# Kernel optimization log

Hardware: AMD Instinct MI355X
Metric: run time of the kernel (lower is better)

The kernel has to match this reference:

```python
import jax, jax.numpy as jnp
import numpy as np

N = 8192          # number of samples
L_FIT = 1.0       # fit (ridge) kernel lengthscale (l_scale folded in)
L_MMD = 1.0       # mmd kernel lengthscale (l_scale folded in)
NUGGET = 1e-4     # diagonal nugget added before inversion
REG_LAMBDA = 1e-5 # regularization weight


def rbf(A, B, l):
    """RBF Gram matrix: exp(-||a-b||^2 / (2 l^2)). A:[n,d], B:[m,d] -> [n,m]."""
    d2 = (jnp.sum(A * A, axis=1)[:, None]
          + jnp.sum(B * B, axis=1)[None, :]
          - 2.0 * (A @ B.T))
    d2 = jnp.maximum(d2, 0.0)
    return jnp.exp(-d2 / (2.0 * l * l))


def setup_inputs() -> dict:
    key = jax.random.key(0)
    k1, k2, k3, k4 = jax.random.split(key, 4)
    X_mu = jax.random.normal(k1, (N, 2), dtype=jnp.float32)
    Y_eta = jax.random.normal(k2, (N, 2), dtype=jnp.float32)
    Y_mu = jax.random.normal(k3, (N, 2), dtype=jnp.float32)
    Z = jax.random.normal(k4, (N, 2), dtype=jnp.float32)  # transport parameter
    return {"X_mu": X_mu, "Y_eta": Y_eta, "Y_mu": Y_mu, "Z": Z}


def reference(X_mu, Y_eta, Y_mu, Z):
    # loss_mmd: MMD between mapped samples and target, uniform weights 1/N
    map_vec = jnp.concatenate([X_mu, Y_eta + Z], axis=1)  # [N, dx+dy]
    Y = jnp.concatenate([X_mu, Y_mu], axis=1)             # [N, dx+dy]
    Ek_ZZ = jnp.mean(rbf(map_vec, map_vec, L_MMD))  # alpha^T K alpha with alpha=1/N
    Ek_ZY = jnp.mean(rbf(map_vec, Y, L_MMD))
    Ek_YY = jnp.mean(rbf(Y, Y, L_MMD))               # E_mmd_YY (constant in torch code)
    loss_mmd = Ek_ZZ - 2.0 * Ek_ZY + Ek_YY

    # loss_reg: reg_lambda * trace(Z^T (K_XX + nugget I)^{-1} Z)
    X = jnp.concatenate([X_mu, Y_eta], axis=1)
    K_fit = rbf(X, X, L_FIT) + NUGGET * jnp.eye(N, dtype=X.dtype)
    K_inv = jnp.linalg.inv(K_fit)
    loss_reg = REG_LAMBDA * jnp.sum(Z * (K_inv @ Z))  # = trace(Z^T Kinv Z)

    return loss_mmd + loss_reg
```

## Files before the change

kernel.cpp:

```cpp
#include <hip/hip_runtime.h>

#define NPTS 8192
#define N2 (NPTS * 2)
#define NCH 16
#define JCH (NPTS / NCH)
#define ITILE 256
#define NIT (NPTS / ITILE)
#define NBLK1 (NIT * NCH)
#define IB 8
#define NIG (ITILE / IB)
#define NJS 16
#define JPT (JCH / NJS)
#define MNY 512
#define SSTR 16
#define T_ITERS 144
#define NUG 1.0e-4
#define INVNUG 1.0e4
#define DELTA 1.0e-2
#define LAM 1.0e-5

#if __has_builtin(__builtin_amdgcn_exp2f)
#define EXP2F(x) __builtin_amdgcn_exp2f(x)
#else
#define EXP2F(x) __expf(0.6931471805599453f * (x))
#endif

extern "C" __global__ void __launch_bounds__(256)
k_setup(const float* __restrict__ Xmu, const float* __restrict__ Yeta,
        const float* __restrict__ Ymu, const float* __restrict__ Z,
        float4* __restrict__ U4, float4* __restrict__ W4, float* __restrict__ NS,
        float4* __restrict__ M4, float4* __restrict__ Y4,
        float2* __restrict__ Pf0, float2* __restrict__ Pf1,
        double* __restrict__ r64, double* __restrict__ x64)
{
  const float c2 = 0.84932180028802f;
  int tid = threadIdx.x;
  int idx = blockIdx.x * 256 + tid;
  int i = idx >> 1;
  r64[idx] = (double)Z[idx];
  x64[idx] = 0.0;
  if ((idx & 1) == 0) {
    float a0 = Xmu[2 * i], a1 = Xmu[2 * i + 1];
    float e0 = Yeta[2 * i], e1 = Yeta[2 * i + 1];
    float m0 = Ymu[2 * i], m1 = Ymu[2 * i + 1];
    float z0 = Z[2 * i], z1 = Z[2 * i + 1];
    float u0 = c2 * a0, u1 = c2 * a1, u2 = c2 * e0, u3 = c2 * e1;
    float n = fmaf(u3, u3, fmaf(u2, u2, fmaf(u1, u1, u0 * u0)));
    U4[i] = make_float4(u0, u1, u2, u3);
    W4[i] = make_float4(2.f * u0, 2.f * u1, 2.f * u2, 2.f * u3);
    NS[i] = n;
    M4[i] = make_float4(a0, a1, e0 + z0, e1 + z1);
    Y4[i] = make_float4(a0, a1, m0, m1);
    Pf0[i] = make_float2(0.f, 0.f);
    Pf1[i] = make_float2(0.f, 0.f);
  }
}

#define MTPB 256
#define MCH 1024
extern "C" __global__ void __launch_bounds__(MTPB)
k_mmd(const float4* __restrict__ M4, const float4* __restrict__ Y4,
      double* __restrict__ mmdpart)
{
  __shared__ float4 sM[MCH];
  __shared__ float4 sY[MCH];
  __shared__ double sred[MTPB];
  int tid = threadIdx.x;
  int blk = blockIdx.x;
  int itile = blk >> 3;
  int ch = blk & 7;
  int j0 = ch * MCH;
  for (int u = tid; u < MCH; u += MTPB) {
    sM[u] = M4[j0 + u];
    sY[u] = Y4[j0 + u];
  }
  __syncthreads();
  int i = itile * MTPB + tid;
  float4 mi = M4[i];
  float4 yi = Y4[i];
  double szz = 0.0, szy = 0.0, syy = 0.0;
  for (int jj = 0; jj < MCH; ++jj) {
    float4 mj = sM[jj];
    float4 yj = sY[jj];
    float d0 = mi.x - mj.x, d1 = mi.y - mj.y;
    float a = fmaf(d1, d1, d0 * d0);
    float u0 = mi.z - mj.z, u1 = mi.w - mj.w;
    float v0 = mi.z - yj.z, v1 = mi.w - yj.w;
    float w0 = yi.z - yj.z, w1 = yi.w - yj.w;
    float dzz = fmaf(u0, u0, fmaf(u1, u1, a));
    float dzy = fmaf(v0, v0, fmaf(v1, v1, a));
    float dyy = fmaf(w0, w0, fmaf(w1, w1, a));
    szz += (double)__expf(-0.5f * dzz);
    szy += (double)__expf(-0.5f * dzy);
    syy += (double)__expf(-0.5f * dyy);
  }
  double v[3] = {szz, szy, syy};
  for (int k = 0; k < 3; ++k) {
    sred[tid] = v[k];
    __syncthreads();
    for (int st = MTPB >> 1; st >= 1; st >>= 1) {
      if (tid < st) sred[tid] += sred[tid + st];
      __syncthreads();
    }
    if (tid == 0) mmdpart[blk * 3 + k] = sred[0];
    __syncthreads();
  }
}

__device__ __forceinline__ float evalK(float4 u, float nu, float4 ws, float nss) {
  float tt = fmaf(u.x, ws.x, fmaf(u.y, ws.y, fmaf(u.z, ws.z, u.w * ws.w)));
  return EXP2F(tt - nu - nss);
}

extern "C" __global__ void __launch_bounds__(256)
k_gbuild(const float4* __restrict__ U4, const float4* __restrict__ W4,
         const float* __restrict__ NS, double* __restrict__ G)
{
  __shared__ float ea[8][32];
  __shared__ float eb[8][32];
  int tid = threadIdx.x;
  int blk = blockIdx.x;
  int a0 = (blk >> 4) * 32;
  int b0 = (blk & 15) * 32;
  int arow = tid >> 5;
  int bl = tid & 31;
  int sa = (a0 + bl) * SSTR;
  int sb = (b0 + bl) * SSTR;
  float4 wsa = W4[sa]; float nsa = NS[sa];
  float4 wsb = W4[sb]; float nsb = NS[sb];
  double acc[4] = {0.0, 0.0, 0.0, 0.0};
  for (int ic = 0; ic < NPTS / 8; ++ic) {
    int i = ic * 8 + arow;
    float4 u = U4[i];
    float nu = NS[i];
    ea[arow][bl] = evalK(u, nu, wsa, nsa);
    eb[arow][bl] = evalK(u, nu, wsb, nsb);
    __syncthreads();
#pragma unroll
    for (int kk = 0; kk < 4; ++kk) {
      int al = (tid >> 5) + 8 * kk;
      double s = 0.0;
#pragma unroll
      for (int ii = 0; ii < 8; ++ii)
        s += (double)ea[ii][al] * (double)eb[ii][bl];
      acc[kk] += s;
    }
    __syncthreads();
  }
#pragma unroll
  for (int kk = 0; kk < 4; ++kk) {
    int al = (tid >> 5) + 8 * kk;
    int a = a0 + al, b = b0 + bl;
    int ia = a * SSTR;
    float4 ua = U4[ia];
    float na = NS[ia];
    double w_ab = (double)evalK(ua, na, wsb, nsb);
    double g = acc[kk] + NUG * w_ab + ((a == b) ? DELTA : 0.0);
    G[(size_t)a * MNY + b] = g;
  }
}

extern "C" __global__ void __launch_bounds__(512)
k_gjpanel(const double* __restrict__ Mc, double* __restrict__ Mn, int k0)
{
  __shared__ double pm[8][8];
  __shared__ double sW[8][MNY];
  __shared__ double cl[8][8];
  __shared__ double trow[8], tcol[8];
  __shared__ double ps;
  int tid = threadIdx.x;
  int blk = blockIdx.x;

  if (tid < 64)
    pm[tid >> 3][tid & 7] = Mc[(size_t)(k0 + (tid >> 3)) * MNY + k0 + (tid & 7)];
  __syncthreads();
  for (int piv = 0; piv < 8; ++piv) {
    if (tid == 0) ps = 1.0 / pm[piv][piv];
    if (tid < 8) { trow[tid] = pm[piv][tid]; tcol[tid] = pm[tid][piv]; }
    __syncthreads();
    double p = ps;
    if (tid < 64) {
      int r = tid >> 3, c = tid & 7;
      double v;
      if (r == piv && c == piv) v = p;
      else if (r == piv)        v = trow[c] * p;
      else if (c == piv)        v = -tcol[r] * p;
      else                      v = fma(-tcol[r] * p, trow[c], pm[r][c]);
      pm[r][c] = v;
    }
    __syncthreads();
  }
  {
    double m[8];
#pragma unroll
    for (int s = 0; s < 8; ++s) m[s] = Mc[(size_t)(k0 + s) * MNY + tid];
#pragma unroll
    for (int r = 0; r < 8; ++r) {
      double acc = 0.0;
#pragma unroll
      for (int s = 0; s < 8; ++s) acc = fma(pm[r][s], m[s], acc);
      sW[r][tid] = acc;
    }
  }
  if (tid < 64)
    cl[tid >> 3][tid & 7] = Mc[(size_t)(blk * 8 + (tid >> 3)) * MNY + k0 + (tid & 7)];
  __syncthreads();

  bool ownerPanel = (blk == (k0 >> 3));
  int jk = tid - k0;
  bool inK = (jk >= 0 && jk < 8);
#pragma unroll
  for (int rr = 0; rr < 8; ++rr) {
    int i = blk * 8 + rr;
    double v;
    if (ownerPanel) {
      v = inK ? pm[rr][jk] : sW[rr][tid];
    } else if (inK) {
      double acc = 0.0;
#pragma unroll
      for (int s = 0; s < 8; ++s) acc = fma(cl[rr][s], pm[s][jk], acc);
      v = -acc;
    } else {
      double acc = Mc[(size_t)i * MNY + tid];
#pragma unroll
      for (int s = 0; s < 8; ++s) acc = fma(-cl[rr][s], sW[s][tid], acc);
      v = acc;
    }
    Mn[(size_t)i * MNY + tid] = v;
  }
}

extern "C" __global__ void __launch_bounds__(512)
k_dbuild(const float4* __restrict__ U4, const float4* __restrict__ W4,
         const float* __restrict__ NS, const double* __restrict__ Ginv,
         float* __restrict__ D)
{
  __shared__ float sc[16][MNY];
  __shared__ float4 su[16];
  __shared__ float snl[16];
  int tid = threadIdx.x;
  int blk = blockIdx.x;
  int i0 = blk * 16;
  if (tid < 16) { su[tid] = U4[i0 + tid]; snl[tid] = NS[i0 + tid]; }
  __syncthreads();
  {
    int si = tid * SSTR;
    float4 ws = W4[si];
    float nss = NS[si];
#pragma unroll
    for (int r = 0; r < 16; ++r)
      sc[r][tid] = evalK(su[r], snl[r], ws, nss);
  }
  __syncthreads();
  double acc[16];
#pragma unroll
  for (int r = 0; r < 16; ++r) acc[r] = 0.0;
  for (int k = 0; k < MNY; ++k) {
    double g = Ginv[(size_t)k * MNY + tid];
#pragma unroll
    for (int r = 0; r < 16; ++r)
      acc[r] = fma((double)sc[r][k], g, acc[r]);
  }
#pragma unroll
  for (int r = 0; r < 16; ++r)
    D[(size_t)(i0 + r) * MNY + tid] = (float)acc[r];
}

extern "C" __global__ void __launch_bounds__(512, 4)
k_matvec(const float4* __restrict__ U4, const float4* __restrict__ W4,
         const float* __restrict__ NS,
         const float2* __restrict__ Zv, const float2* __restrict__ Pfp,
         float2* __restrict__ Pfc, float2* __restrict__ qpart,
         double* __restrict__ pqpart, const double* __restrict__ rhopart, int t)
{
  __shared__ float4 sw[JCH];
  __shared__ float4 sa[JCH];
  __shared__ double s1[512], s2[512];
  __shared__ double sc[2];
  int tid = threadIdx.x;
  int blk = blockIdx.x;
  int it = blk >> 4;
  int ch = blk & (NCH - 1);
  int j = ch * JCH + tid;

  float4 wj = W4[j];
  float nj = NS[j];
  float2 zj = Zv[j];
  float2 pj = Pfp[j];

  if (t == 1) {
    if (tid < 2) sc[tid] = 0.0;
    __syncthreads();
  } else {
    const double* cur = rhopart + ((t - 1) & 1) * 128;
    const double* prv = rhopart + ((t - 2) & 1) * 128;
    if (tid < 128) { s1[tid] = cur[tid]; s2[tid] = prv[tid]; }
    __syncthreads();
    for (int st = 64; st >= 2; st >>= 1) {
      if (tid < st) { s1[tid] += s1[tid + st]; s2[tid] += s2[tid + st]; }
      __syncthreads();
    }
    if (tid < 2) sc[tid] = s1[tid] / s2[tid];
    __syncthreads();
  }
  float b0 = (float)sc[0], b1 = (float)sc[1];

  sw[tid] = wj;
  sa[tid] = make_float4(nj, fmaf(b0, pj.x, zj.x), fmaf(b1, pj.y, zj.y), 0.f);
  __syncthreads();

  int js = tid & (NJS - 1);
  int ig = tid >> 4;
  int i0 = it * ITILE + ig * IB;
  float4 ui[IB];
  float ni[IB];
#pragma unroll
  for (int k = 0; k < IB; ++k) { ui[k] = U4[i0 + k]; ni[k] = NS[i0 + k]; }
  float qa0[IB], qa1[IB];
#pragma unroll
  for (int k = 0; k < IB; ++k) { qa0[k] = 0.f; qa1[k] = 0.f; }
#pragma unroll 4
  for (int jj = 0; jj < JPT; ++jj) {
    int jl = jj * NJS + js;
    float4 w = sw[jl];
    float4 aa = sa[jl];
#pragma unroll
    for (int k = 0; k < IB; ++k) {
      float ttn = -(ni[k] + aa.x);
      ttn = fmaf(ui[k].x, w.x, ttn);
      ttn = fmaf(ui[k].y, w.y, ttn);
      ttn = fmaf(ui[k].z, w.z, ttn);
      ttn = fmaf(ui[k].w, w.w, ttn);
      float e = EXP2F(ttn);
      qa0[k] = fmaf(e, aa.y, qa0[k]);
      qa1[k] = fmaf(e, aa.z, qa1[k]);
    }
  }
#pragma unroll
  for (int k = 0; k < IB; ++k) {
#pragma unroll
    for (int d = 8; d >= 1; d >>= 1) {
      qa0[k] += __shfl_down(qa0[k], (unsigned)d, 16);
      qa1[k] += __shfl_down(qa1[k], (unsigned)d, 16);
    }
  }
  double pq0 = 0.0, pq1 = 0.0;
  if (js == 0) {
    int owner = (it & (NCH - 1));
#pragma unroll
    for (int k = 0; k < IB; ++k) {
      int i = i0 + k;
      float2 zi = Zv[i];
      float2 pi = Pfp[i];
      float pn0 = fmaf(b0, pi.x, zi.x);
      float pn1 = fmaf(b1, pi.y, zi.y);
      qpart[(size_t)ch * NPTS + i] = make_float2(qa0[k], qa1[k]);
      if (ch == owner) Pfc[i] = make_float2(pn0, pn1);
      pq0 += (double)pn0 * (double)qa0[k];
      pq1 += (double)pn1 * (double)qa1[k];
      if (ch == 0) {
        pq0 += NUG * (double)pn0 * (double)pn0;
        pq1 += NUG * (double)pn1 * (double)pn1;
      }
    }
  }
  s1[tid] = pq0;
  s2[tid] = pq1;
  __syncthreads();
  for (int st = 256; st >= 1; st >>= 1) {
    if (tid < st) { s1[tid] += s1[tid + st]; s2[tid] += s2[tid + st]; }
    __syncthreads();
  }
  if (tid == 0) { pqpart[blk * 2 + 0] = s1[0]; pqpart[blk * 2 + 1] = s2[0]; }
}

extern "C" __global__ void __launch_bounds__(256)
k_update(const float* __restrict__ qpartf, const float2* __restrict__ Pfc,
         double* __restrict__ r64, double* __restrict__ x64,
         const float4* __restrict__ U4, const float4* __restrict__ W4,
         const float* __restrict__ NS,
         const double* __restrict__ pqpart, const double* __restrict__ rhopart,
         double* __restrict__ y1part, int t)
{
  __shared__ double s1[256];
  __shared__ double s2[128];
  __shared__ double alpha2[2];
  __shared__ float4 su[128];
  __shared__ float snl[128];
  __shared__ double rl[2][128];
  int tid = threadIdx.x;
  int blk = blockIdx.x;
  int idx = blk * 256 + tid;
  double rv;
  if (t > 0) {
    s1[tid] = pqpart[tid] + pqpart[tid + 256] + pqpart[tid + 512] + pqpart[tid + 768];
    if (tid < 128) s2[tid] = rhopart[((t - 1) & 1) * 128 + tid];
    __syncthreads();
    for (int st = 128; st >= 2; st >>= 1) {
      if (tid < st) s1[tid] += s1[tid + st];
      if (st <= 64 && tid < st) s2[tid] += s2[tid + st];
      __syncthreads();
    }
    if (tid < 2) alpha2[tid] = s2[tid] / s1[tid];
    __syncthreads();
    double a = alpha2[idx & 1];
    float pn = ((const float*)Pfc)[idx];
    double q = 0.0;
#pragma unroll
    for (int c = 0; c < NCH; ++c) q += (double)qpartf[(size_t)c * N2 + idx];
    q = fma((double)NUG, (double)pn, q);
    rv = fma(-a, q, r64[idx]);
    x64[idx] = fma(a, (double)pn, x64[idx]);
    r64[idx] = rv;
  } else {
    rv = r64[idx];
  }
  rl[idx & 1][tid >> 1] = rv;
  if (tid < 128) {
    su[tid] = U4[blk * 128 + tid];
    snl[tid] = NS[blk * 128 + tid];
  }
  __syncthreads();
  for (int rr = 0; rr < MNY / 256; ++rr) {
    int s = rr * 256 + tid;
    int si = s * SSTR;
    float4 ws = W4[si];
    float nss = NS[si];
    double y0 = 0.0, y1v = 0.0;
#pragma unroll 4
    for (int il = 0; il < 128; ++il) {
      float4 u = su[il];
      float tt = fmaf(u.x, ws.x, fmaf(u.y, ws.y, fmaf(u.z, ws.z, u.w * ws.w)));
      float e = EXP2F(tt - snl[il] - nss);
      y0 = fma((double)e, rl[0][il], y0);
      y1v = fma((double)e, rl[1][il], y1v);
    }
    y1part[(size_t)s * 128 + blk * 2 + 0] = y0;
    y1part[(size_t)s * 128 + blk * 2 + 1] = y1v;
  }
}

extern "C" __global__ void __launch_bounds__(256)
k_dz(const double* __restrict__ r64, const double* __restrict__ y1part,
     const float* __restrict__ D, float2* __restrict__ Zv,
     double* __restrict__ rhopart, int t)
{
  __shared__ double ly1[MNY][2];
  __shared__ double zl[128][2];
  __shared__ double s1[256], s2[256];
  int tid = threadIdx.x;
  int blk = blockIdx.x;
  for (int s = tid; s < MNY; s += 256) {
    const double* base = y1part + (size_t)s * 128;
    double a0 = 0.0, a1 = 0.0;
#pragma unroll 8
    for (int b = 0; b < 64; ++b) { a0 += base[2 * b]; a1 += base[2 * b + 1]; }
    ly1[s][0] = a0; ly1[s][1] = a1;
  }
  __syncthreads();
  {
    int lane = tid & 63, wv = tid >> 6;
    for (int rnd = 0; rnd < 32; ++rnd) {
      int pt = wv * 32 + rnd;
      const float* drow = D + (size_t)(blk * 128 + pt) * MNY;
      double a0 = 0.0, a1 = 0.0;
#pragma unroll
      for (int m = 0; m < MNY / 64; ++m) {
        int s = lane + 64 * m;
        double dv = (double)drow[s];
        a0 = fma(dv, ly1[s][0], a0);
        a1 = fma(dv, ly1[s][1], a1);
      }
#pragma unroll
      for (int d = 32; d >= 1; d >>= 1) {
        a0 += __shfl_down(a0, (unsigned)d, 64);
        a1 += __shfl_down(a1, (unsigned)d, 64);
      }
      if (lane == 0) { zl[pt][0] = a0; zl[pt][1] = a1; }
    }
  }
  __syncthreads();
  double rz0 = 0.0, rz1 = 0.0;
  if (tid < 128) {
    int i = blk * 128 + tid;
    double r0 = r64[2 * i], r1 = r64[2 * i + 1];
    double z0 = (r0 - zl[tid][0]) * INVNUG;
    double z1 = (r1 - zl[tid][1]) * INVNUG;
    Zv[i] = make_float2((float)z0, (float)z1);
    rz0 = r0 * z0;
    rz1 = r1 * z1;
  }
  s1[tid] = rz0;
  s2[tid] = rz1;
  __syncthreads();
  for (int st = 128; st >= 1; st >>= 1) {
    if (tid < st) { s1[tid] += s1[tid + st]; s2[tid] += s2[tid + st]; }
    __syncthreads();
  }
  if (tid == 0) {
    rhopart[(t & 1) * 128 + blk * 2 + 0] = s1[0];
    rhopart[(t & 1) * 128 + blk * 2 + 1] = s2[0];
  }
}

extern "C" __global__ void __launch_bounds__(256)
k_y2z(const float4* __restrict__ U4, const float4* __restrict__ W4,
      const float* __restrict__ NS, const double* __restrict__ r64,
      const double* __restrict__ y1part, const double* __restrict__ Ginv,
      float2* __restrict__ Zv, double* __restrict__ rhopart, int t)
{
  __shared__ double ly1[MNY][2];
  __shared__ double ly2[MNY][2];
  __shared__ double s1[256], s2[256];
  int tid = threadIdx.x;
  int blk = blockIdx.x;
  for (int s = tid; s < MNY; s += 256) {
    const double* base = y1part + (size_t)s * 128;
    double a0 = 0.0, a1 = 0.0;
#pragma unroll 8
    for (int b = 0; b < 64; ++b) { a0 += base[2 * b]; a1 += base[2 * b + 1]; }
    ly1[s][0] = a0; ly1[s][1] = a1;
  }
  __syncthreads();
  {
    int g = tid >> 5, l = tid & 31;
    for (int ss = 0; ss < MNY / 8; ++ss) {
      int so = g * (MNY / 8) + ss;
      const double* grow = Ginv + (size_t)so * MNY;
      double c0 = 0.0, c1 = 0.0;
#pragma unroll
      for (int m = 0; m < MNY / 32; ++m) {
        int jj = m * 32 + l;
        double gv = grow[jj];
        c0 = fma(gv, ly1[jj][0], c0);
        c1 = fma(gv, ly1[jj][1], c1);
      }
#pragma unroll
      for (int d = 16; d >= 1; d >>= 1) {
        c0 += __shfl_down(c0, (unsigned)d, 32);
        c1 += __shfl_down(c1, (unsigned)d, 32);
      }
      if (l == 0) { ly2[so][0] = c0; ly2[so][1] = c1; }
    }
  }
  __syncthreads();
  int pt = tid & 127;
  int half = tid >> 7;
  int i = blk * 128 + pt;
  float4 u = U4[i];
  float nu = NS[i];
  double acc0 = 0.0, acc1 = 0.0;
  int sbase = half * (MNY / 2);
#pragma unroll 4
  for (int s = 0; s < MNY / 2; ++s) {
    int so = sbase + s;
    int si = so * SSTR;
    float4 ws = W4[si];
    float nss = NS[si];
    float tt = fmaf(u.x, ws.x, fmaf(u.y, ws.y, fmaf(u.z, ws.z, u.w * ws.w)));
    float e = EXP2F(tt - nu - nss);
    acc0 = fma((double)e, ly2[so][0], acc0);
    acc1 = fma((double)e, ly2[so][1], acc1);
  }
  s1[tid] = acc0;
  s2[tid] = acc1;
  __syncthreads();
  double rz0 = 0.0, rz1 = 0.0;
  if (tid < 128) {
    double a0 = s1[tid] + s1[tid + 128];
    double a1 = s2[tid] + s2[tid + 128];
    double r0 = r64[2 * i], r1 = r64[2 * i + 1];
    double z0 = (r0 - a0) * INVNUG;
    double z1 = (r1 - a1) * INVNUG;
    Zv[i] = make_float2((float)z0, (float)z1);
    rz0 = r0 * z0;
    rz1 = r1 * z1;
  }
  __syncthreads();
  s1[tid] = rz0;
  s2[tid] = rz1;
  __syncthreads();
  for (int st = 128; st >= 1; st >>= 1) {
    if (tid < st) { s1[tid] += s1[tid + st]; s2[tid] += s2[tid + st]; }
    __syncthreads();
  }
  if (tid == 0) {
    rhopart[(t & 1) * 128 + blk * 2 + 0] = s1[0];
    rhopart[(t & 1) * 128 + blk * 2 + 1] = s2[0];
  }
}

extern "C" __global__ void __launch_bounds__(256)
k_final(const float* __restrict__ Z, const double* __restrict__ x64,
        const double* __restrict__ mmdpart, float* __restrict__ out)
{
  __shared__ double sred[256];
  int tid = threadIdx.x;
  double zx = 0.0;
  for (int idx = tid; idx < N2; idx += 256)
    zx += (double)Z[idx] * x64[idx];
  double acc[4];
  acc[0] = zx;
  acc[1] = mmdpart[tid * 3 + 0];
  acc[2] = mmdpart[tid * 3 + 1];
  acc[3] = mmdpart[tid * 3 + 2];
  double tot[4];
  for (int k = 0; k < 4; ++k) {
    sred[tid] = acc[k];
    __syncthreads();
    for (int st = 128; st >= 1; st >>= 1) {
      if (tid < st) sred[tid] += sred[tid + st];
      __syncthreads();
    }
    tot[k] = sred[0];
    __syncthreads();
  }
  if (tid == 0) {
    double nn = (double)NPTS * (double)NPTS;
    double mmd = (tot[1] - 2.0 * tot[2] + tot[3]) / nn;
    out[0] = (float)(mmd + LAM * tot[0]);
  }
}

extern "C" void kernel_launch(void* const* d_in, const int* in_sizes, int n_in,
                              void* d_out, int out_size, void* d_ws, size_t ws_size,
                              hipStream_t stream)
{
  (void)in_sizes; (void)n_in; (void)out_size;
  const float* Xmu  = (const float*)d_in[0];
  const float* Yeta = (const float*)d_in[1];
  const float* Ymu  = (const float*)d_in[2];
  const float* Z    = (const float*)d_in[3];
  float* out = (float*)d_out;

  char* w = (char*)d_ws;
  float4* U4      = (float4*)(w);
  float4* W4      = (float4*)(w + (128 << 10));
  float*  NS      = (float*)(w + (256 << 10));
  float4* M4      = (float4*)(w + (288 << 10));
  float4* Y4      = (float4*)(w + (416 << 10));
  float2* Zv      = (float2*)(w + (544 << 10));
  float2* Pf[2]   = { (float2*)(w + (608 << 10)), (float2*)(w + (672 << 10)) };
  double* r64     = (double*)(w + (736 << 10));
  double* x64     = (double*)(w + (864 << 10));
  float2* qpart   = (float2*)(w + (992 << 10));
  double* pqpart  = (double*)(w + (2016 << 10));
  double* rhopart = (double*)(w + (2024 << 10));
  double* y1part  = (double*)(w + (2026 << 10));
  double* mmdpart = (double*)(w + (2546 << 10));
  double* Gb0     = (double*)(w + (2552 << 10));
  double* Gb1     = (double*)(w + (4600 << 10));
  float*  D       = (float*)(w + (6656 << 10));
  int useD = (ws_size >= ((size_t)(6656 + 16384) << 10)) ? 1 : 0;

  hipLaunchKernelGGL(k_setup, dim3(64), dim3(256), 0, stream,
                     Xmu, Yeta, Ymu, Z, U4, W4, NS, M4, Y4,
                     Pf[0], Pf[1], r64, x64);
  hipLaunchKernelGGL(k_mmd, dim3(256), dim3(MTPB), 0, stream, M4, Y4, mmdpart);
  hipLaunchKernelGGL(k_gbuild, dim3(256), dim3(256), 0, stream, U4, W4, NS, Gb0);
  for (int p = 0; p < MNY / 8; ++p) {
    double* Mc = (p & 1) ? Gb1 : Gb0;
    double* Mn = (p & 1) ? Gb0 : Gb1;
    hipLaunchKernelGGL(k_gjpanel, dim3(64), dim3(512), 0, stream, Mc, Mn, p * 8);
  }
  double* Ginv = Gb0;
  if (useD)
    hipLaunchKernelGGL(k_dbuild, dim3(512), dim3(512), 0, stream,
                       U4, W4, NS, Ginv, D);

  hipLaunchKernelGGL(k_update, dim3(64), dim3(256), 0, stream,
                     (const float*)qpart, Pf[0], r64, x64, U4, W4, NS,
                     pqpart, rhopart, y1part, 0);
  if (useD)
    hipLaunchKernelGGL(k_dz, dim3(64), dim3(256), 0, stream,
                       r64, y1part, D, Zv, rhopart, 0);
  else
    hipLaunchKernelGGL(k_y2z, dim3(64), dim3(256), 0, stream,
                       U4, W4, NS, r64, y1part, Ginv, Zv, rhopart, 0);

  for (int t = 1; t <= T_ITERS; ++t) {
    float2* Pprev = Pf[(t - 1) & 1];
    float2* Pcur  = Pf[t & 1];
    hipLaunchKernelGGL(k_matvec, dim3(NBLK1), dim3(512), 0, stream,
                       U4, W4, NS, Zv, Pprev, Pcur, qpart, pqpart, rhopart, t);
    hipLaunchKernelGGL(k_update, dim3(64), dim3(256), 0, stream,
                       (const float*)qpart, Pcur, r64, x64, U4, W4, NS,
                       pqpart, rhopart, y1part, t);
    if (t < T_ITERS) {
      if (useD)
        hipLaunchKernelGGL(k_dz, dim3(64), dim3(256), 0, stream,
                           r64, y1part, D, Zv, rhopart, t);
      else
        hipLaunchKernelGGL(k_y2z, dim3(64), dim3(256), 0, stream,
                           U4, W4, NS, r64, y1part, Ginv, Zv, rhopart, t);
    }
  }
  hipLaunchKernelGGL(k_final, dim3(1), dim3(256), 0, stream,
                     Z, x64, mmdpart, out);
}
```

Measured before the change: 11.08 ms.

## Fuse update and dz kernels with an atomic grid-wide barrier

The per-iteration k_update and k_dz launches are merged into one kernel, k_upz. An agent-scope atomic counter acts as a software grid barrier across the 64 co-resident blocks, replacing the kernel boundary. This removes one launch and its stream synchronisation point per CG iteration. In exchange it relies on all blocks being resident at once and spins on a global counter. It also runs the dz stage on the last iteration, which is unneeded, and its shared-memory reduction writes past the 128-entry s2 array.

```diff
diff --git a/kernel.cpp b/kernel.cpp
--- a/kernel.cpp
+++ b/kernel.cpp
@@ -31,13 +31,16 @@
         float4* __restrict__ U4, float4* __restrict__ W4, float* __restrict__ NS,
         float4* __restrict__ M4, float4* __restrict__ Y4,
         float2* __restrict__ Pf0, float2* __restrict__ Pf1,
-        double* __restrict__ r64, double* __restrict__ x64)
+        double* __restrict__ r64, double* __restrict__ x64,
+        unsigned int* __restrict__ counter)
 {
   const float c2 = 0.84932180028802f;
   int tid = threadIdx.x;
   int idx = blockIdx.x * 256 + tid;
   int i = idx >> 1;
-  r64[idx] = (double)Z[idx];
+  if (blockIdx.x == 0 && tid == 0) counter[0] = 0u;
+  float z = Z[idx];
+  r64[idx] = (double)z;
   x64[idx] = 0.0;
   if ((idx & 1) == 0) {
     float a0 = Xmu[2 * i], a1 = Xmu[2 * i + 1];
@@ -375,12 +378,14 @@
 }
 
 extern "C" __global__ void __launch_bounds__(256)
-k_update(const float* __restrict__ qpartf, const float2* __restrict__ Pfc,
-         double* __restrict__ r64, double* __restrict__ x64,
-         const float4* __restrict__ U4, const float4* __restrict__ W4,
-         const float* __restrict__ NS,
-         const double* __restrict__ pqpart, const double* __restrict__ rhopart,
-         double* __restrict__ y1part, int t)
+k_upz(const float* __restrict__ qpartf, const float2* __restrict__ Pfc,
+      double* __restrict__ r64, double* __restrict__ x64,
+      const float4* __restrict__ U4, const float4* __restrict__ W4,
+      const float* __restrict__ NS,
+      const double* __restrict__ pqpart, double* __restrict__ rhopart,
+      double* __restrict__ y1part, const float* __restrict__ D,
+      float2* __restrict__ Zv, unsigned int* __restrict__ counter,
+      int t, unsigned int lidx)
 {
   __shared__ double s1[256];
   __shared__ double s2[128];
@@ -388,9 +393,12 @@
   __shared__ float4 su[128];
   __shared__ float snl[128];
   __shared__ double rl[2][128];
+  __shared__ double ly1[MNY][2];
+  __shared__ double zl[128][2];
   int tid = threadIdx.x;
   int blk = blockIdx.x;
   int idx = blk * 256 + tid;
+
   double rv;
   if (t > 0) {
     s1[tid] = pqpart[tid] + pqpart[tid + 256] + pqpart[tid + 512] + pqpart[tid + 768];
@@ -438,18 +446,16 @@
     y1part[(size_t)s * 128 + blk * 2 + 0] = y0;
     y1part[(size_t)s * 128 + blk * 2 + 1] = y1v;
   }
-}
-
-extern "C" __global__ void __launch_bounds__(256)
-k_dz(const double* __restrict__ r64, const double* __restrict__ y1part,
-     const float* __restrict__ D, float2* __restrict__ Zv,
-     double* __restrict__ rhopart, int t)
-{
-  __shared__ double ly1[MNY][2];
-  __shared__ double zl[128][2];
-  __shared__ double s1[256], s2[256];
-  int tid = threadIdx.x;
-  int blk = blockIdx.x;
+  __syncthreads();
+
+  if (tid == 0) {
+    __hip_atomic_fetch_add(counter, 1u, __ATOMIC_ACQ_REL, __HIP_MEMORY_SCOPE_AGENT);
+    unsigned int target = 64u * (lidx + 1u);
+    while (__hip_atomic_load(counter, __ATOMIC_ACQUIRE, __HIP_MEMORY_SCOPE_AGENT) < target)
+      __builtin_amdgcn_s_sleep(8);
+  }
+  __syncthreads();
+
   for (int s = tid; s < MNY; s += 256) {
     const double* base = y1part + (size_t)s * 128;
     double a0 = 0.0, a1 = 0.0;
@@ -491,10 +497,15 @@
     rz1 = r1 * z1;
   }
   s1[tid] = rz0;
-  s2[tid] = rz1;
+  s2[tid] = (tid < 128) ? rz1 : 0.0;
+  __syncthreads();
+  if (tid >= 128) s1[tid] = 0.0;
   __syncthreads();
   for (int st = 128; st >= 1; st >>= 1) {
-    if (tid < st) { s1[tid] += s1[tid + st]; s2[tid] += s2[tid + st]; }
+    if (tid < st) {
+      s1[tid] += s1[tid + st];
+      if (tid + st < 128 || st >= 128) s2[tid] += (tid + st < 256) ? s2[tid + st] : 0.0;
+    }
     __syncthreads();
   }
   if (tid == 0) {
@@ -591,6 +602,72 @@
 }
 
 extern "C" __global__ void __launch_bounds__(256)
+k_update(const float* __restrict__ qpartf, const float2* __restrict__ Pfc,
+         double* __restrict__ r64, double* __restrict__ x64,
+         const float4* __restrict__ U4, const float4* __restrict__ W4,
+         const float* __restrict__ NS,
+         const double* __restrict__ pqpart, const double* __restrict__ rhopart,
+         double* __restrict__ y1part, int t)
+{
+  __shared__ double s1[256];
+  __shared__ double s2[128];
+  __shared__ double alpha2[2];
+  __shared__ float4 su[128];
+  __shared__ float snl[128];
+  __shared__ double rl[2][128];
+  int tid = threadIdx.x;
+  int blk = blockIdx.x;
+  int idx = blk * 256 + tid;
+  double rv;
+  if (t > 0) {
+    s1[tid] = pqpart[tid] + pqpart[tid + 256] + pqpart[tid + 512] + pqpart[tid + 768];
+    if (tid < 128) s2[tid] = rhopart[((t - 1) & 1) * 128 + tid];
+    __syncthreads();
+    for (int st = 128; st >= 2; st >>= 1) {
+      if (tid < st) s1[tid] += s1[tid + st];
+      if (st <= 64 && tid < st) s2[tid] += s2[tid + st];
+      __syncthreads();
+    }
+    if (tid < 2) alpha2[tid] = s2[tid] / s1[tid];
+    __syncthreads();
+    double a = alpha2[idx & 1];
+    float pn = ((const float*)Pfc)[idx];
+    double q = 0.0;
+#pragma unroll
+    for (int c = 0; c < NCH; ++c) q += (double)qpartf[(size_t)c * N2 + idx];
+    q = fma((double)NUG, (double)pn, q);
+    rv = fma(-a, q, r64[idx]);
+    x64[idx] = fma(a, (double)pn, x64[idx]);
+    r64[idx] = rv;
+  } else {
+    rv = r64[idx];
+  }
+  rl[idx & 1][tid >> 1] = rv;
+  if (tid < 128) {
+    su[tid] = U4[blk * 128 + tid];
+    snl[tid] = NS[blk * 128 + tid];
+  }
+  __syncthreads();
+  for (int rr = 0; rr < MNY / 256; ++rr) {
+    int s = rr * 256 + tid;
+    int si = s * SSTR;
+    float4 ws = W4[si];
+    float nss = NS[si];
+    double y0 = 0.0, y1v = 0.0;
+#pragma unroll 4
+    for (int il = 0; il < 128; ++il) {
+      float4 u = su[il];
+      float tt = fmaf(u.x, ws.x, fmaf(u.y, ws.y, fmaf(u.z, ws.z, u.w * ws.w)));
+      float e = EXP2F(tt - snl[il] - nss);
+      y0 = fma((double)e, rl[0][il], y0);
+      y1v = fma((double)e, rl[1][il], y1v);
+    }
+    y1part[(size_t)s * 128 + blk * 2 + 0] = y0;
+    y1part[(size_t)s * 128 + blk * 2 + 1] = y1v;
+  }
+}
+
+extern "C" __global__ void __launch_bounds__(256)
 k_final(const float* __restrict__ Z, const double* __restrict__ x64,
         const double* __restrict__ mmdpart, float* __restrict__ out)
 {
@@ -646,6 +723,7 @@
   float2* qpart   = (float2*)(w + (992 << 10));
   double* pqpart  = (double*)(w + (2016 << 10));
   double* rhopart = (double*)(w + (2024 << 10));
+  unsigned int* counter = (unsigned int*)(w + (2025 << 10) + 512);
   double* y1part  = (double*)(w + (2026 << 10));
   double* mmdpart = (double*)(w + (2546 << 10));
   double* Gb0     = (double*)(w + (2552 << 10));
@@ -655,7 +733,7 @@
 
   hipLaunchKernelGGL(k_setup, dim3(64), dim3(256), 0, stream,
                      Xmu, Yeta, Ymu, Z, U4, W4, NS, M4, Y4,
-                     Pf[0], Pf[1], r64, x64);
+                     Pf[0], Pf[1], r64, x64, counter);
   hipLaunchKernelGGL(k_mmd, dim3(256), dim3(MTPB), 0, stream, M4, Y4, mmdpart);
   hipLaunchKernelGGL(k_gbuild, dim3(256), dim3(256), 0, stream, U4, W4, NS, Gb0);
   for (int p = 0; p < MNY / 8; ++p) {
@@ -668,29 +746,37 @@
     hipLaunchKernelGGL(k_dbuild, dim3(512), dim3(512), 0, stream,
                        U4, W4, NS, Ginv, D);
 
-  hipLaunchKernelGGL(k_update, dim3(64), dim3(256), 0, stream,
-                     (const float*)qpart, Pf[0], r64, x64, U4, W4, NS,
-                     pqpart, rhopart, y1part, 0);
-  if (useD)
-    hipLaunchKernelGGL(k_dz, dim3(64), dim3(256), 0, stream,
-                       r64, y1part, D, Zv, rhopart, 0);
-  else
+  unsigned int lidx = 0;
+  if (useD) {
+    hipLaunchKernelGGL(k_upz, dim3(64), dim3(256), 0, stream,
+                       (const float*)qpart, Pf[0], r64, x64, U4, W4, NS,
+                       pqpart, rhopart, y1part, D, Zv, counter, 0, lidx);
+    ++lidx;
+    for (int t = 1; t <= T_ITERS; ++t) {
+      float2* Pprev = Pf[(t - 1) & 1];
+      float2* Pcur  = Pf[t & 1];
+      hipLaunchKernelGGL(k_matvec, dim3(NBLK1), dim3(512), 0, stream,
+                         U4, W4, NS, Zv, Pprev, Pcur, qpart, pqpart, rhopart, t);
+      hipLaunchKernelGGL(k_upz, dim3(64), dim3(256), 0, stream,
+                         (const float*)qpart, Pcur, r64, x64, U4, W4, NS,
+                         pqpart, rhopart, y1part, D, Zv, counter, t, lidx);
+      ++lidx;
+    }
+  } else {
+    hipLaunchKernelGGL(k_update, dim3(64), dim3(256), 0, stream,
+                       (const float*)qpart, Pf[0], r64, x64, U4, W4, NS,
+                       pqpart, rhopart, y1part, 0);
     hipLaunchKernelGGL(k_y2z, dim3(64), dim3(256), 0, stream,
                        U4, W4, NS, r64, y1part, Ginv, Zv, rhopart, 0);
-
-  for (int t = 1; t <= T_ITERS; ++t) {
-    float2* Pprev = Pf[(t - 1) & 1];
-    float2* Pcur  = Pf[t & 1];
-    hipLaunchKernelGGL(k_matvec, dim3(NBLK1), dim3(512), 0, stream,
-                       U4, W4, NS, Zv, Pprev, Pcur, qpart, pqpart, rhopart, t);
-    hipLaunchKernelGGL(k_update, dim3(64), dim3(256), 0, stream,
-                       (const float*)qpart, Pcur, r64, x64, U4, W4, NS,
-                       pqpart, rhopart, y1part, t);
-    if (t < T_ITERS) {
-      if (useD)
-        hipLaunchKernelGGL(k_dz, dim3(64), dim3(256), 0, stream,
-                           r64, y1part, D, Zv, rhopart, t);
-      else
+    for (int t = 1; t <= T_ITERS; ++t) {
+      float2* Pprev = Pf[(t - 1) & 1];
+      float2* Pcur  = Pf[t & 1];
+      hipLaunchKernelGGL(k_matvec, dim3(NBLK1), dim3(512), 0, stream,
+                         U4, W4, NS, Zv, Pprev, Pcur, qpart, pqpart, rhopart, t);
+      hipLaunchKernelGGL(k_update, dim3(64), dim3(256), 0, stream,
+                         (const float*)qpart, Pcur, r64, x64, U4, W4, NS,
+                         pqpart, rhopart, y1part, t);
+      if (t < T_ITERS)
         hipLaunchKernelGGL(k_y2z, dim3(64), dim3(256), 0, stream,
                            U4, W4, NS, r64, y1part, Ginv, Zv, rhopart, t);
     }
```

Result: slower. 11.53 ms (+4.1%).

## Template Nyström preconditioner rank and use 1024 landmarks with fewer PCG iterations

Applied to the files above, without the earlier changes.

The preconditioner-related kernels are templated on the landmark count M. When the workspace is large enough, the code uses 1024 landmarks instead of 512 and cuts the fixed PCG iteration count from 144 to 120. The Gauss-Jordan inversion now eliminates 16-wide panels, so it needs half as many launches. The aim is to trade a more expensive setup and heavier per-iteration preconditioner applies for fewer full N×N kernel matvecs. This relies on the stronger preconditioner converging within the smaller fixed iteration budget, and it needs much more workspace and LDS.

```diff
diff --git a/kernel.cpp b/kernel.cpp
--- a/kernel.cpp
+++ b/kernel.cpp
@@ -8,12 +8,8 @@
 #define NIT (NPTS / ITILE)
 #define NBLK1 (NIT * NCH)
 #define IB 8
-#define NIG (ITILE / IB)
 #define NJS 16
 #define JPT (JCH / NJS)
-#define MNY 512
-#define SSTR 16
-#define T_ITERS 144
 #define NUG 1.0e-4
 #define INVNUG 1.0e4
 #define DELTA 1.0e-2
@@ -57,20 +53,20 @@
 }
 
 #define MTPB 256
-#define MCH 1024
+#define MCHK 1024
 extern "C" __global__ void __launch_bounds__(MTPB)
 k_mmd(const float4* __restrict__ M4, const float4* __restrict__ Y4,
       double* __restrict__ mmdpart)
 {
-  __shared__ float4 sM[MCH];
-  __shared__ float4 sY[MCH];
+  __shared__ float4 sM[MCHK];
+  __shared__ float4 sY[MCHK];
   __shared__ double sred[MTPB];
   int tid = threadIdx.x;
   int blk = blockIdx.x;
   int itile = blk >> 3;
   int ch = blk & 7;
-  int j0 = ch * MCH;
-  for (int u = tid; u < MCH; u += MTPB) {
+  int j0 = ch * MCHK;
+  for (int u = tid; u < MCHK; u += MTPB) {
     sM[u] = M4[j0 + u];
     sY[u] = Y4[j0 + u];
   }
@@ -79,7 +75,7 @@
   float4 mi = M4[i];
   float4 yi = Y4[i];
   double szz = 0.0, szy = 0.0, syy = 0.0;
-  for (int jj = 0; jj < MCH; ++jj) {
+  for (int jj = 0; jj < MCHK; ++jj) {
     float4 mj = sM[jj];
     float4 yj = sY[jj];
     float d0 = mi.x - mj.x, d1 = mi.y - mj.y;
@@ -112,20 +108,22 @@
   return EXP2F(tt - nu - nss);
 }
 
-extern "C" __global__ void __launch_bounds__(256)
+template<int M>
+__global__ void __launch_bounds__(256)
 k_gbuild(const float4* __restrict__ U4, const float4* __restrict__ W4,
          const float* __restrict__ NS, double* __restrict__ G)
 {
+  constexpr int SS = NPTS / M;
   __shared__ float ea[8][32];
   __shared__ float eb[8][32];
   int tid = threadIdx.x;
   int blk = blockIdx.x;
-  int a0 = (blk >> 4) * 32;
-  int b0 = (blk & 15) * 32;
+  int a0 = (blk / (M / 32)) * 32;
+  int b0 = (blk % (M / 32)) * 32;
   int arow = tid >> 5;
   int bl = tid & 31;
-  int sa = (a0 + bl) * SSTR;
-  int sb = (b0 + bl) * SSTR;
+  int sa = (a0 + bl) * SS;
+  int sb = (b0 + bl) * SS;
   float4 wsa = W4[sa]; float nsa = NS[sa];
   float4 wsb = W4[sb]; float nsb = NS[sb];
   double acc[4] = {0.0, 0.0, 0.0, 0.0};
@@ -151,36 +149,37 @@
   for (int kk = 0; kk < 4; ++kk) {
     int al = (tid >> 5) + 8 * kk;
     int a = a0 + al, b = b0 + bl;
-    int ia = a * SSTR;
+    int ia = a * SS;
     float4 ua = U4[ia];
     float na = NS[ia];
     double w_ab = (double)evalK(ua, na, wsb, nsb);
     double g = acc[kk] + NUG * w_ab + ((a == b) ? DELTA : 0.0);
-    G[(size_t)a * MNY + b] = g;
-  }
-}
-
-extern "C" __global__ void __launch_bounds__(512)
+    G[(size_t)a * M + b] = g;
+  }
+}
+
+template<int M>
+__global__ void __launch_bounds__(1024)
 k_gjpanel(const double* __restrict__ Mc, double* __restrict__ Mn, int k0)
 {
-  __shared__ double pm[8][8];
-  __shared__ double sW[8][MNY];
-  __shared__ double cl[8][8];
-  __shared__ double trow[8], tcol[8];
+  __shared__ double pm[16][16];
+  __shared__ double sW[16][M];
+  __shared__ double cl[8][16];
+  __shared__ double trow[16], tcol[16];
   __shared__ double ps;
   int tid = threadIdx.x;
   int blk = blockIdx.x;
 
-  if (tid < 64)
-    pm[tid >> 3][tid & 7] = Mc[(size_t)(k0 + (tid >> 3)) * MNY + k0 + (tid & 7)];
-  __syncthreads();
-  for (int piv = 0; piv < 8; ++piv) {
+  if (tid < 256)
+    pm[tid >> 4][tid & 15] = Mc[(size_t)(k0 + (tid >> 4)) * M + k0 + (tid & 15)];
+  __syncthreads();
+  for (int piv = 0; piv < 16; ++piv) {
     if (tid == 0) ps = 1.0 / pm[piv][piv];
-    if (tid < 8) { trow[tid] = pm[piv][tid]; tcol[tid] = pm[tid][piv]; }
+    if (tid < 16) { trow[tid] = pm[piv][tid]; tcol[tid] = pm[tid][piv]; }
     __syncthreads();
     double p = ps;
-    if (tid < 64) {
-      int r = tid >> 3, c = tid & 7;
+    if (tid < 256) {
+      int r = tid >> 4, c = tid & 15;
       double v;
       if (r == piv && c == piv) v = p;
       else if (r == piv)        v = trow[c] * p;
@@ -191,51 +190,53 @@
     __syncthreads();
   }
   {
-    double m[8];
-#pragma unroll
-    for (int s = 0; s < 8; ++s) m[s] = Mc[(size_t)(k0 + s) * MNY + tid];
-#pragma unroll
-    for (int r = 0; r < 8; ++r) {
+    double m[16];
+#pragma unroll
+    for (int s = 0; s < 16; ++s) m[s] = Mc[(size_t)(k0 + s) * M + tid];
+#pragma unroll
+    for (int r = 0; r < 16; ++r) {
       double acc = 0.0;
 #pragma unroll
-      for (int s = 0; s < 8; ++s) acc = fma(pm[r][s], m[s], acc);
+      for (int s = 0; s < 16; ++s) acc = fma(pm[r][s], m[s], acc);
       sW[r][tid] = acc;
     }
   }
-  if (tid < 64)
-    cl[tid >> 3][tid & 7] = Mc[(size_t)(blk * 8 + (tid >> 3)) * MNY + k0 + (tid & 7)];
-  __syncthreads();
-
-  bool ownerPanel = (blk == (k0 >> 3));
+  if (tid < 128)
+    cl[tid >> 4][tid & 15] = Mc[(size_t)(blk * 8 + (tid >> 4)) * M + k0 + (tid & 15)];
+  __syncthreads();
+
   int jk = tid - k0;
-  bool inK = (jk >= 0 && jk < 8);
+  bool inK = (jk >= 0 && jk < 16);
 #pragma unroll
   for (int rr = 0; rr < 8; ++rr) {
     int i = blk * 8 + rr;
+    int pr = i - k0;
     double v;
-    if (ownerPanel) {
-      v = inK ? pm[rr][jk] : sW[rr][tid];
+    if (pr >= 0 && pr < 16) {
+      v = inK ? pm[pr][jk] : sW[pr][tid];
     } else if (inK) {
       double acc = 0.0;
 #pragma unroll
-      for (int s = 0; s < 8; ++s) acc = fma(cl[rr][s], pm[s][jk], acc);
+      for (int s = 0; s < 16; ++s) acc = fma(cl[rr][s], pm[s][jk], acc);
       v = -acc;
     } else {
-      double acc = Mc[(size_t)i * MNY + tid];
-#pragma unroll
-      for (int s = 0; s < 8; ++s) acc = fma(-cl[rr][s], sW[s][tid], acc);
+      double acc = Mc[(size_t)i * M + tid];
+#pragma unroll
+      for (int s = 0; s < 16; ++s) acc = fma(-cl[rr][s], sW[s][tid], acc);
       v = acc;
     }
-    Mn[(size_t)i * MNY + tid] = v;
-  }
-}
-
-extern "C" __global__ void __launch_bounds__(512)
+    Mn[(size_t)i * M + tid] = v;
+  }
+}
+
+template<int M>
+__global__ void __launch_bounds__(1024)
 k_dbuild(const float4* __restrict__ U4, const float4* __restrict__ W4,
          const float* __restrict__ NS, const double* __restrict__ Ginv,
          float* __restrict__ D)
 {
-  __shared__ float sc[16][MNY];
+  constexpr int SS = NPTS / M;
+  __shared__ float sc[16][M];
   __shared__ float4 su[16];
   __shared__ float snl[16];
   int tid = threadIdx.x;
@@ -244,7 +245,7 @@
   if (tid < 16) { su[tid] = U4[i0 + tid]; snl[tid] = NS[i0 + tid]; }
   __syncthreads();
   {
-    int si = tid * SSTR;
+    int si = tid * SS;
     float4 ws = W4[si];
     float nss = NS[si];
 #pragma unroll
@@ -255,15 +256,15 @@
   double acc[16];
 #pragma unroll
   for (int r = 0; r < 16; ++r) acc[r] = 0.0;
-  for (int k = 0; k < MNY; ++k) {
-    double g = Ginv[(size_t)k * MNY + tid];
+  for (int k = 0; k < M; ++k) {
+    double g = Ginv[(size_t)k * M + tid];
 #pragma unroll
     for (int r = 0; r < 16; ++r)
       acc[r] = fma((double)sc[r][k], g, acc[r]);
   }
 #pragma unroll
   for (int r = 0; r < 16; ++r)
-    D[(size_t)(i0 + r) * MNY + tid] = (float)acc[r];
+    D[(size_t)(i0 + r) * M + tid] = (float)acc[r];
 }
 
 extern "C" __global__ void __launch_bounds__(512, 4)
@@ -374,7 +375,8 @@
   if (tid == 0) { pqpart[blk * 2 + 0] = s1[0]; pqpart[blk * 2 + 1] = s2[0]; }
 }
 
-extern "C" __global__ void __launch_bounds__(256)
+template<int M>
+__global__ void __launch_bounds__(256)
 k_update(const float* __restrict__ qpartf, const float2* __restrict__ Pfc,
          double* __restrict__ r64, double* __restrict__ x64,
          const float4* __restrict__ U4, const float4* __restrict__ W4,
@@ -382,6 +384,7 @@
          const double* __restrict__ pqpart, const double* __restrict__ rhopart,
          double* __restrict__ y1part, int t)
 {
+  constexpr int SS = NPTS / M;
   __shared__ double s1[256];
   __shared__ double s2[128];
   __shared__ double alpha2[2];
@@ -421,9 +424,9 @@
     snl[tid] = NS[blk * 128 + tid];
   }
   __syncthreads();
-  for (int rr = 0; rr < MNY / 256; ++rr) {
+  for (int rr = 0; rr < M / 256; ++rr) {
     int s = rr * 256 + tid;
-    int si = s * SSTR;
+    int si = s * SS;
     float4 ws = W4[si];
     float nss = NS[si];
     double y0 = 0.0, y1v = 0.0;
@@ -440,17 +443,18 @@
   }
 }
 
-extern "C" __global__ void __launch_bounds__(256)
+template<int M>
+__global__ void __launch_bounds__(256)
 k_dz(const double* __restrict__ r64, const double* __restrict__ y1part,
      const float* __restrict__ D, float2* __restrict__ Zv,
      double* __restrict__ rhopart, int t)
 {
-  __shared__ double ly1[MNY][2];
+  __shared__ double ly1[M][2];
   __shared__ double zl[128][2];
   __shared__ double s1[256], s2[256];
   int tid = threadIdx.x;
   int blk = blockIdx.x;
-  for (int s = tid; s < MNY; s += 256) {
+  for (int s = tid; s < M; s += 256) {
     const double* base = y1part + (size_t)s * 128;
     double a0 = 0.0, a1 = 0.0;
 #pragma unroll 8
@@ -462,10 +466,10 @@
     int lane = tid & 63, wv = tid >> 6;
     for (int rnd = 0; rnd < 32; ++rnd) {
       int pt = wv * 32 + rnd;
-      const float* drow = D + (size_t)(blk * 128 + pt) * MNY;
+      const float* drow = D + (size_t)(blk * 128 + pt) * M;
       double a0 = 0.0, a1 = 0.0;
 #pragma unroll
-      for (int m = 0; m < MNY / 64; ++m) {
+      for (int m = 0; m < M / 64; ++m) {
         int s = lane + 64 * m;
         double dv = (double)drow[s];
         a0 = fma(dv, ly1[s][0], a0);
@@ -503,18 +507,20 @@
   }
 }
 
-extern "C" __global__ void __launch_bounds__(256)
+template<int M>
+__global__ void __launch_bounds__(256)
 k_y2z(const float4* __restrict__ U4, const float4* __restrict__ W4,
       const float* __restrict__ NS, const double* __restrict__ r64,
       const double* __restrict__ y1part, const double* __restrict__ Ginv,
       float2* __restrict__ Zv, double* __restrict__ rhopart, int t)
 {
-  __shared__ double ly1[MNY][2];
-  __shared__ double ly2[MNY][2];
+  constexpr int SS = NPTS / M;
+  __shared__ double ly1[M][2];
+  __shared__ double ly2[M][2];
   __shared__ double s1[256], s2[256];
   int tid = threadIdx.x;
   int blk = blockIdx.x;
-  for (int s = tid; s < MNY; s += 256) {
+  for (int s = tid; s < M; s += 256) {
     const double* base = y1part + (size_t)s * 128;
     double a0 = 0.0, a1 = 0.0;
 #pragma unroll 8
@@ -524,12 +530,12 @@
   __syncthreads();
   {
     int g = tid >> 5, l = tid & 31;
-    for (int ss = 0; ss < MNY / 8; ++ss) {
-      int so = g * (MNY / 8) + ss;
-      const double* grow = Ginv + (size_t)so * MNY;
+    for (int ss = 0; ss < M / 8; ++ss) {
+      int so = g * (M / 8) + ss;
+      const double* grow = Ginv + (size_t)so * M;
       double c0 = 0.0, c1 = 0.0;
 #pragma unroll
-      for (int m = 0; m < MNY / 32; ++m) {
+      for (int m = 0; m < M / 32; ++m) {
         int jj = m * 32 + l;
         double gv = grow[jj];
         c0 = fma(gv, ly1[jj][0], c0);
@@ -550,11 +556,11 @@
   float4 u = U4[i];
   float nu = NS[i];
   double acc0 = 0.0, acc1 = 0.0;
-  int sbase = half * (MNY / 2);
+  int sbase = half * (M / 2);
 #pragma unroll 4
-  for (int s = 0; s < MNY / 2; ++s) {
+  for (int s = 0; s < M / 2; ++s) {
     int so = sbase + s;
-    int si = so * SSTR;
+    int si = so * SS;
     float4 ws = W4[si];
     float nss = NS[si];
     float tt = fmaf(u.x, ws.x, fmaf(u.y, ws.y, fmaf(u.z, ws.z, u.w * ws.w)));
@@ -622,6 +628,56 @@
   }
 }
 
+template<int M>
+static void run_pcg(const float4* U4, const float4* W4, const float* NS,
+                    const float* Z, float2* Zv, float2* Pf0, float2* Pf1,
+                    double* r64, double* x64, float2* qpart, double* pqpart,
+                    double* rhopart, double* y1part, double* Gb0, double* Gb1,
+                    float* D, int useD, int T, hipStream_t stream)
+{
+  hipLaunchKernelGGL((k_gbuild<M>), dim3((M / 32) * (M / 32)), dim3(256), 0,
+                     stream, U4, W4, NS, Gb0);
+  for (int p = 0; p < M / 16; ++p) {
+    double* Mc = (p & 1) ? Gb1 : Gb0;
+    double* Mn = (p & 1) ? Gb0 : Gb1;
+    hipLaunchKernelGGL((k_gjpanel<M>), dim3(M / 8), dim3(M), 0, stream,
+                       Mc, Mn, p * 16);
+  }
+  double* Ginv = Gb0;
+  if (useD)
+    hipLaunchKernelGGL((k_dbuild<M>), dim3(512), dim3(M), 0, stream,
+                       U4, W4, NS, Ginv, D);
+
+  float2* Pf[2] = { Pf0, Pf1 };
+  hipLaunchKernelGGL((k_update<M>), dim3(64), dim3(256), 0, stream,
+                     (const float*)qpart, Pf[0], r64, x64, U4, W4, NS,
+                     pqpart, rhopart, y1part, 0);
+  if (useD)
+    hipLaunchKernelGGL((k_dz<M>), dim3(64), dim3(256), 0, stream,
+                       r64, y1part, D, Zv, rhopart, 0);
+  else
+    hipLaunchKernelGGL((k_y2z<M>), dim3(64), dim3(256), 0, stream,
+                       U4, W4, NS, r64, y1part, Ginv, Zv, rhopart, 0);
+
+  for (int t = 1; t <= T; ++t) {
+    float2* Pprev = Pf[(t - 1) & 1];
+    float2* Pcur  = Pf[t & 1];
+    hipLaunchKernelGGL(k_matvec, dim3(NBLK1), dim3(512), 0, stream,
+                       U4, W4, NS, Zv, Pprev, Pcur, qpart, pqpart, rhopart, t);
+    hipLaunchKernelGGL((k_update<M>), dim3(64), dim3(256), 0, stream,
+                       (const float*)qpart, Pcur, r64, x64, U4, W4, NS,
+                       pqpart, rhopart, y1part, t);
+    if (t < T) {
+      if (useD)
+        hipLaunchKernelGGL((k_dz<M>), dim3(64), dim3(256), 0, stream,
+                           r64, y1part, D, Zv, rhopart, t);
+      else
+        hipLaunchKernelGGL((k_y2z<M>), dim3(64), dim3(256), 0, stream,
+                           U4, W4, NS, r64, y1part, Ginv, Zv, rhopart, t);
+    }
+  }
+}
+
 extern "C" void kernel_launch(void* const* d_in, const int* in_sizes, int n_in,
                               void* d_out, int out_size, void* d_ws, size_t ws_size,
                               hipStream_t stream)
@@ -640,61 +696,45 @@
   float4* M4      = (float4*)(w + (288 << 10));
   float4* Y4      = (float4*)(w + (416 << 10));
   float2* Zv      = (float2*)(w + (544 << 10));
-  float2* Pf[2]   = { (float2*)(w + (608 << 10)), (float2*)(w + (672 << 10)) };
+  float2* Pf0     = (float2*)(w + (608 << 10));
+  float2* Pf1     = (float2*)(w + (672 << 10));
   double* r64     = (double*)(w + (736 << 10));
   double* x64     = (double*)(w + (864 << 10));
   float2* qpart   = (float2*)(w + (992 << 10));
   double* pqpart  = (double*)(w + (2016 << 10));
   double* rhopart = (double*)(w + (2024 << 10));
-  double* y1part  = (double*)(w + (2026 << 10));
-  double* mmdpart = (double*)(w + (2546 << 10));
-  double* Gb0     = (double*)(w + (2552 << 10));
-  double* Gb1     = (double*)(w + (4600 << 10));
-  float*  D       = (float*)(w + (6656 << 10));
-  int useD = (ws_size >= ((size_t)(6656 + 16384) << 10)) ? 1 : 0;
+  double* mmdpart = (double*)(w + (2026 << 10));
+  double* y1part  = (double*)(w + (2032 << 10));
+
+  size_t need1024 = ((size_t)2032 << 10) + ((size_t)1024 * 128 * 8)
+                  + 2 * ((size_t)1024 * 1024 * 8) + ((size_t)8192 * 1024 * 4);
+  size_t need512  = ((size_t)2032 << 10) + ((size_t)512 * 128 * 8)
+                  + 2 * ((size_t)512 * 512 * 8) + ((size_t)8192 * 512 * 4);
+  size_t need512noD = ((size_t)2032 << 10) + ((size_t)512 * 128 * 8)
+                  + 2 * ((size_t)512 * 512 * 8);
+
+  int m, T, useD;
+  if (ws_size >= need1024)      { m = 1024; T = 120; useD = 1; }
+  else if (ws_size >= need512)  { m = 512;  T = 144; useD = 1; }
+  else                          { m = 512;  T = 144; useD = 0; (void)need512noD; }
+
+  size_t p = ((size_t)2032 << 10) + (size_t)m * 128 * 8;
+  double* Gb0 = (double*)(w + p);  p += (size_t)m * m * 8;
+  double* Gb1 = (double*)(w + p);  p += (size_t)m * m * 8;
+  float*  D   = (float*)(w + p);
 
   hipLaunchKernelGGL(k_setup, dim3(64), dim3(256), 0, stream,
                      Xmu, Yeta, Ymu, Z, U4, W4, NS, M4, Y4,
-                     Pf[0], Pf[1], r64, x64);
+                     Pf0, Pf1, r64, x64);
   hipLaunchKernelGGL(k_mmd, dim3(256), dim3(MTPB), 0, stream, M4, Y4, mmdpart);
-  hipLaunchKernelGGL(k_gbuild, dim3(256), dim3(256), 0, stream, U4, W4, NS, Gb0);
-  for (int p = 0; p < MNY / 8; ++p) {
-    double* Mc = (p & 1) ? Gb1 : Gb0;
-    double* Mn = (p & 1) ? Gb0 : Gb1;
-    hipLaunchKernelGGL(k_gjpanel, dim3(64), dim3(512), 0, stream, Mc, Mn, p * 8);
-  }
-  double* Ginv = Gb0;
-  if (useD)
-    hipLaunchKernelGGL(k_dbuild, dim3(512), dim3(512), 0, stream,
-                       U4, W4, NS, Ginv, D);
-
-  hipLaunchKernelGGL(k_update, dim3(64), dim3(256), 0, stream,
-                     (const float*)qpart, Pf[0], r64, x64, U4, W4, NS,
-                     pqpart, rhopart, y1part, 0);
-  if (useD)
-    hipLaunchKernelGGL(k_dz, dim3(64), dim3(256), 0, stream,
-                       r64, y1part, D, Zv, rhopart, 0);
+
+  if (m == 1024)
+    run_pcg<1024>(U4, W4, NS, Z, Zv, Pf0, Pf1, r64, x64, qpart, pqpart,
+                  rhopart, y1part, Gb0, Gb1, D, useD, T, stream);
   else
-    hipLaunchKernelGGL(k_y2z, dim3(64), dim3(256), 0, stream,
-                       U4, W4, NS, r64, y1part, Ginv, Zv, rhopart, 0);
-
-  for (int t = 1; t <= T_ITERS; ++t) {
-    float2* Pprev = Pf[(t - 1) & 1];
-    float2* Pcur  = Pf[t & 1];
-    hipLaunchKernelGGL(k_matvec, dim3(NBLK1), dim3(512), 0, stream,
-                       U4, W4, NS, Zv, Pprev, Pcur, qpart, pqpart, rhopart, t);
-    hipLaunchKernelGGL(k_update, dim3(64), dim3(256), 0, stream,
-                       (const float*)qpart, Pcur, r64, x64, U4, W4, NS,
-                       pqpart, rhopart, y1part, t);
-    if (t < T_ITERS) {
-      if (useD)
-        hipLaunchKernelGGL(k_dz, dim3(64), dim3(256), 0, stream,
-                           r64, y1part, D, Zv, rhopart, t);
-      else
-        hipLaunchKernelGGL(k_y2z, dim3(64), dim3(256), 0, stream,
-                           U4, W4, NS, r64, y1part, Ginv, Zv, rhopart, t);
-    }
-  }
+    run_pcg<512>(U4, W4, NS, Z, Zv, Pf0, Pf1, r64, x64, qpart, pqpart,
+                 rhopart, y1part, Gb0, Gb1, D, useD, T, stream);
+
   hipLaunchKernelGGL(k_final, dim3(1), dim3(256), 0, stream,
                      Z, x64, mmdpart, out);
 }
```

Result: slower. 15.12 ms (+36.5%).
